# Kernel optimization log

Measured on AMD Instinct MI355X. Metric: run time of the kernel, lower is better.

## Reference

```python
import jax, jax.numpy as jnp
import numpy as np

B, T, F, H, OUT = 256, 256, 128, 1024, 128


def setup_inputs() -> dict:
    key = jax.random.key(0)
    ks = jax.random.split(key, 6)
    s_ih = 1.0 / np.sqrt(H)
    return {
        "x": jax.random.normal(ks[0], (B, T, F), dtype=jnp.float32),
        "h0": jnp.zeros((B, H), dtype=jnp.float32),
        "c0": jnp.zeros((B, H), dtype=jnp.float32),
        "W_ih": jax.random.normal(ks[1], (4 * H, F), dtype=jnp.float32) * s_ih,
        "W_hh": jax.random.normal(ks[2], (4 * H, H), dtype=jnp.float32) * s_ih,
        "b_ih": jax.random.normal(ks[3], (4 * H,), dtype=jnp.float32) * s_ih,
        "b_hh": jax.random.normal(ks[4], (4 * H,), dtype=jnp.float32) * s_ih,
        "W_fc": jax.random.normal(ks[5], (OUT, H), dtype=jnp.float32) * s_ih,
        "b_fc": jnp.zeros((OUT,), dtype=jnp.float32),
    }


def _lstm_scan(x, h0, c0, W_ih, W_hh, b_ih, b_hh):
    # Precompute input projections for all timesteps: [T, B, 4H]
    x_t = jnp.swapaxes(x, 0, 1)  # [T, B, F]
    x_proj = jnp.einsum('tbf,gf->tbg', x_t, W_ih) + b_ih + b_hh

    def step(carry, xp):
        h, c = carry
        gates = xp + h @ W_hh.T  # [B, 4H]
        i, f, g, o = jnp.split(gates, 4, axis=-1)  # PyTorch LSTMCell gate order
        i = jax.nn.sigmoid(i)
        f = jax.nn.sigmoid(f)
        g = jnp.tanh(g)
        o = jax.nn.sigmoid(o)
        c = f * c + i * g
        h = o * jnp.tanh(c)
        return (h, c), None

    (h, c), _ = jax.lax.scan(step, (h0, c0), x_proj)
    return h, c


def reference(x, h0, c0, W_ih, W_hh, b_ih, b_hh, W_fc, b_fc):
    h, c = _lstm_scan(x, h0, c0, W_ih, W_hh, b_ih, b_hh)
    sig_out = jax.nn.sigmoid(h)
    # Dropout is identity in eval/reference mode
    return sig_out @ W_fc.T + b_fc  # [B, OUT]
```

## Files before the change

### kernel.cpp

```cpp
#include <hip/hip_runtime.h>


typedef _Float16 f16x8 __attribute__((ext_vector_type(8)));
typedef float f32x16 __attribute__((ext_vector_type(16)));
typedef unsigned long long u64;

#define SCOPE_AGENT __HIP_MEMORY_SCOPE_AGENT

#define WS_WP    0ull
#define WS_BIAS  9437184ull
#define WS_XT    (WS_BIAS + 16384ull)
#define WS_HB    (WS_XT + 16777216ull)
#define WS_SIGH  (WS_HB + 4ull * 524288ull)
#define WS_BAR   (WS_SIGH + 1048576ull)

__device__ __forceinline__ unsigned short f2h(float f) {
  _Float16 h = (_Float16)f;
  return __builtin_bit_cast(unsigned short, h);
}

__device__ __forceinline__ float fast_sig(float x) {
  return __builtin_amdgcn_rcpf(1.f + __expf(-x));
}
__device__ __forceinline__ float fast_tanh(float x) {
  return __builtin_fmaf(2.f, fast_sig(2.f * x), -1.f);
}

__global__ void prep_pack(const float* __restrict__ W_ih, const float* __restrict__ W_hh,
                          const float* __restrict__ b_ih, const float* __restrict__ b_hh,
                          unsigned short* __restrict__ wp, float* __restrict__ bias) {
  unsigned i = blockIdx.x * 256u + threadIdx.x;
  if (i < 4718592u) {
    unsigned j = i & 7u;
    unsigned l = (i >> 3) & 63u;
    unsigned rest = i >> 9;
    unsigned q = rest % 18u;
    unsigned rest2 = rest / 18u;
    unsigned n = rest2 & 3u;
    unsigned rest3 = rest2 >> 2;
    unsigned w = rest3 & 3u;
    unsigned cg = rest3 >> 2;
    unsigned gcol = n * 1024u + cg * 32u + (l & 31u);
    unsigned khi = (l >> 5) * 8u + j;
    float v;
    if (q < 16u) {
      unsigned k = w * 256u + q * 16u + khi;
      v = W_hh[(size_t)gcol * 1024u + k];
    } else {
      unsigned k = w * 32u + (q - 16u) * 16u + khi;
      v = W_ih[(size_t)gcol * 128u + k];
    }
    wp[i] = f2h(v);
  }
  if (i < 4096u) bias[i] = b_ih[i] + b_hh[i];
}

__global__ void prep_misc(const float* __restrict__ x, const float* __restrict__ h0,
                          unsigned short* __restrict__ xT, unsigned short* __restrict__ hb0,
                          unsigned* __restrict__ bar) {
  unsigned i = blockIdx.x * 256u + threadIdx.x;
  if (i < 8388608u) {
    unsigned f = i & 127u;
    unsigned b = (i >> 7) & 255u;
    unsigned t = i >> 15;
    xT[i] = f2h(x[((size_t)b * 256u + t) * 128u + f]);
  }
  if (i < 262144u) hb0[i] = f2h(h0[i]);
  if (i < 768u) bar[i] = 0u;
}

__launch_bounds__(256, 1)
__global__ void lstm_main(const unsigned short* __restrict__ wp,
                          const float* __restrict__ bias,
                          const unsigned short* __restrict__ xT,
                          unsigned short* __restrict__ hb,
                          const float* __restrict__ c0,
                          float* __restrict__ sigh,
                          unsigned* __restrict__ bar) {
  extern __shared__ char lds[];
  float4* redv = (float4*)(lds + 65536);
  unsigned short* hst = (unsigned short*)(lds + 131072);

  const unsigned tid = threadIdx.x;
  const unsigned wg  = blockIdx.x;
  const unsigned w   = tid >> 6;
  const unsigned l   = tid & 63u;
  const unsigned rg  = wg >> 5;
  const unsigned cg  = wg & 31u;
  const unsigned lo5 = l & 31u;
  const unsigned hi  = l >> 5;

  int4 Braw[4][18];
  {
    const int4* wpv = (const int4*)wp;
    const unsigned wbase = (cg * 4u + w) * 4608u;
#pragma unroll
    for (int n = 0; n < 4; ++n) {
#pragma unroll
      for (int q = 0; q < 18; ++q) {
        Braw[n][q] = wpv[wbase + (unsigned)(n * 18 + q) * 64u + l];
      }
    }
  }

  float bias_v[4];
#pragma unroll
  for (int n = 0; n < 4; ++n) bias_v[n] = bias[(unsigned)n * 1024u + cg * 32u + lo5];

  const unsigned col = cg * 32u + lo5;
  float c_st[4];
  unsigned soff[4];
#pragma unroll
  for (int i = 0; i < 4; ++i) {
    unsigned r = rg * 32u + 8u * w + (unsigned)i + 4u * hi;
    soff[i] = r * 1024u + col;
    c_st[i] = c0[soff[i]];
  }

  const unsigned sgsrc0 = (rg * 32u + hi) * 2048u + w * 512u + lo5 * 16u;
  const unsigned sdst0  = w * 16384u + hi * 512u + lo5 * 16u;
  const unsigned fbase = w * 16384u + lo5 * 512u + hi * 16u;
  const unsigned fxor  = (lo5 & 7u) << 4;

  unsigned xb = ((rg * 32u + lo5) * 128u + w * 32u + hi * 8u) * 2u;

  const char* xbase = (const char*)xT;
  const char* hbase = (const char*)hb;
  unsigned* flags = &bar[rg * 32u];

  const unsigned srow = tid >> 3;
  const unsigned sseg = tid & 7u;
  const unsigned sgoff = (((rg * 32u + srow) * 1024u) + cg * 32u + sseg * 4u) * 2u;

  int4 xr[2];
  xr[0] = *(const int4*)(xbase + xb);
  xr[1] = *(const int4*)(xbase + xb + 32u);

  for (unsigned t = 0; t < 256u; ++t) {
    const char* hrd = hbase + ((t & 3u) * 524288u);
    char* hwr = (char*)hbase + (((t + 1u) & 3u) * 524288u);

    u64 sa[16], sb[16];
#pragma unroll
    for (int r = 0; r < 16; ++r) {
      const char* src = hrd + sgsrc0 + (unsigned)r * 4096u;
      sa[r] = __hip_atomic_load((const u64*)src,       __ATOMIC_RELAXED, SCOPE_AGENT);
      sb[r] = __hip_atomic_load((const u64*)(src + 8), __ATOMIC_RELAXED, SCOPE_AGENT);
    }

    f32x16 acc[4] = {};
#pragma unroll
    for (int qx = 0; qx < 2; ++qx) {
      f16x8 a = __builtin_bit_cast(f16x8, xr[qx]);
      acc[0] = __builtin_amdgcn_mfma_f32_32x32x16_f16(a, __builtin_bit_cast(f16x8, Braw[0][16 + qx]), acc[0], 0, 0, 0);
      acc[1] = __builtin_amdgcn_mfma_f32_32x32x16_f16(a, __builtin_bit_cast(f16x8, Braw[1][16 + qx]), acc[1], 0, 0, 0);
      acc[2] = __builtin_amdgcn_mfma_f32_32x32x16_f16(a, __builtin_bit_cast(f16x8, Braw[2][16 + qx]), acc[2], 0, 0, 0);
      acc[3] = __builtin_amdgcn_mfma_f32_32x32x16_f16(a, __builtin_bit_cast(f16x8, Braw[3][16 + qx]), acc[3], 0, 0, 0);
    }

#pragma unroll
    for (int r = 0; r < 16; ++r) {
      unsigned d = sdst0 + (unsigned)r * 1024u;
      unsigned a = d ^ (((d >> 9) & 7u) << 4);
      struct { u64 a, b; } p = { sa[r], sb[r] };
      *(int4*)(lds + a) = __builtin_bit_cast(int4, p);
    }
    asm volatile("s_waitcnt lgkmcnt(0)" ::: "memory");

#pragma unroll
    for (int q = 0; q < 16; ++q) {
      int4 av = *(const int4*)(lds + ((fbase + (unsigned)q * 32u) ^ fxor));
      f16x8 a = __builtin_bit_cast(f16x8, av);
      acc[0] = __builtin_amdgcn_mfma_f32_32x32x16_f16(a, __builtin_bit_cast(f16x8, Braw[0][q]), acc[0], 0, 0, 0);
      acc[1] = __builtin_amdgcn_mfma_f32_32x32x16_f16(a, __builtin_bit_cast(f16x8, Braw[1][q]), acc[1], 0, 0, 0);
      acc[2] = __builtin_amdgcn_mfma_f32_32x32x16_f16(a, __builtin_bit_cast(f16x8, Braw[2][q]), acc[2], 0, 0, 0);
      acc[3] = __builtin_amdgcn_mfma_f32_32x32x16_f16(a, __builtin_bit_cast(f16x8, Braw[3][q]), acc[3], 0, 0, 0);
    }

#pragma unroll
    for (int n = 0; n < 4; ++n) {
#pragma unroll
      for (int c = 0; c < 4; ++c) {
        float4 v;
        v.x = acc[n][4 * c + 0]; v.y = acc[n][4 * c + 1];
        v.z = acc[n][4 * c + 2]; v.w = acc[n][4 * c + 3];
        redv[((w * 4u + (unsigned)n) * 4u + (unsigned)c) * 64u + l] = v;
      }
    }
    __syncthreads();

    float gv[4][4];
#pragma unroll
    for (int n = 0; n < 4; ++n) {
      float4 s; s.x = bias_v[n]; s.y = bias_v[n]; s.z = bias_v[n]; s.w = bias_v[n];
#pragma unroll
      for (int wo = 0; wo < 4; ++wo) {
        float4 v = redv[(((unsigned)wo * 4u + (unsigned)n) * 4u + w) * 64u + l];
        s.x += v.x; s.y += v.y; s.z += v.z; s.w += v.w;
      }
      gv[n][0] = s.x; gv[n][1] = s.y; gv[n][2] = s.z; gv[n][3] = s.w;
    }

    const bool last = (t == 255u);
#pragma unroll
    for (int i = 0; i < 4; ++i) {
      float ig = fast_sig(gv[0][i]);
      float fg = fast_sig(gv[1][i]);
      float gg = fast_tanh(gv[2][i]);
      float og = fast_sig(gv[3][i]);
      float cc = fg * c_st[i] + ig * gg;
      c_st[i] = cc;
      float hh = og * fast_tanh(cc);
      hst[(8u * w + (unsigned)i + 4u * hi) * 32u + lo5] = f2h(hh);
      if (last) sigh[soff[i]] = fast_sig(hh);
    }

    if (!last) {
      __syncthreads();
      {
        u64 v = *(const u64*)(hst + srow * 32u + sseg * 4u);
        __hip_atomic_store((u64*)(hwr + sgoff), v, __ATOMIC_RELAXED, SCOPE_AGENT);
      }
      xb += 65536u;
      xr[0] = *(const int4*)(xbase + xb);
      xr[1] = *(const int4*)(xbase + xb + 32u);
      __syncthreads();
      if (tid == 0)
        __hip_atomic_store(&flags[cg], t + 1u, __ATOMIC_RELAXED, SCOPE_AGENT);
      {
        const unsigned tgt = t + 1u;
        const unsigned fidx = w * 8u + (l & 7u);
        for (;;) {
          unsigned f = __hip_atomic_load(&flags[fidx], __ATOMIC_RELAXED, SCOPE_AGENT);
          if (__all(l >= 8u || f >= tgt)) break;
          __builtin_amdgcn_s_sleep(1);
        }
      }
    }
  }
}

__global__ void final_fc(const float* __restrict__ sigh, const float* __restrict__ W_fc,
                         const float* __restrict__ b_fc, float* __restrict__ out) {
  unsigned b = blockIdx.x;
  unsigned o = threadIdx.x;
  const float* hrow = sigh + (size_t)b * 1024u;
  const float* wrow = W_fc + (size_t)o * 1024u;
  float acc = b_fc[o];
#pragma unroll 8
  for (unsigned k = 0; k < 1024u; k += 4u) {
    float4 hv = *(const float4*)(hrow + k);
    float4 wv = *(const float4*)(wrow + k);
    acc += hv.x * wv.x + hv.y * wv.y + hv.z * wv.z + hv.w * wv.w;
  }
  out[b * 128u + o] = acc;
}

extern "C" void kernel_launch(void* const* d_in, const int* in_sizes, int n_in,
                              void* d_out, int out_size, void* d_ws, size_t ws_size,
                              hipStream_t stream) {
  (void)in_sizes; (void)n_in; (void)out_size; (void)ws_size;
  const float* x    = (const float*)d_in[0];
  const float* h0   = (const float*)d_in[1];
  const float* c0   = (const float*)d_in[2];
  const float* W_ih = (const float*)d_in[3];
  const float* W_hh = (const float*)d_in[4];
  const float* b_ih = (const float*)d_in[5];
  const float* b_hh = (const float*)d_in[6];
  const float* W_fc = (const float*)d_in[7];
  const float* b_fc = (const float*)d_in[8];

  char* ws = (char*)d_ws;
  unsigned short* wp   = (unsigned short*)(ws + WS_WP);
  float*          bias = (float*)(ws + WS_BIAS);
  unsigned short* xT   = (unsigned short*)(ws + WS_XT);
  unsigned short* hb   = (unsigned short*)(ws + WS_HB);
  float*          sigh = (float*)(ws + WS_SIGH);
  unsigned*       bar  = (unsigned*)(ws + WS_BAR);
  float*          out  = (float*)d_out;

  prep_pack<<<18432, 256, 0, stream>>>(W_ih, W_hh, b_ih, b_hh, wp, bias);
  prep_misc<<<32768, 256, 0, stream>>>(x, h0, xT, hb, bar);
  lstm_main<<<256, 256, 133120, stream>>>(wp, bias, xT, hb, c0, sigh, bar);
  final_fc<<<256, 128, 0, stream>>>(sigh, W_fc, b_fc, out);
}
```

Before: 1.307 ms.

## Double waves per block, store h in MFMA fragment layout, drop LDS staging

Each workgroup now runs 8 waves instead of 4, so each wave handles half the K range with half the register-resident weights. The shared h buffer is stored directly in MFMA A-fragment layout, so waves load fragments from global memory without the LDS transpose, and the next fragments are prefetched while MFMAs run. The cross-wave reduction grows to 8 partials, and each thread applies the gate math to 2 rows. The flag polling also changes so all lanes check flags. The aim is more latency hiding and a shorter serial per-step path, at the cost of a larger reduction and smaller stores per thread.

```diff
diff --git a/kernel.cpp b/kernel.cpp
--- a/kernel.cpp
+++ b/kernel.cpp
@@ -4,6 +4,7 @@
 typedef _Float16 f16x8 __attribute__((ext_vector_type(8)));
 typedef float f32x16 __attribute__((ext_vector_type(16)));
 typedef unsigned long long u64;
+struct U128 { u64 a, b; };
 
 #define SCOPE_AGENT __HIP_MEMORY_SCOPE_AGENT
 
@@ -24,6 +25,13 @@
 }
 __device__ __forceinline__ float fast_tanh(float x) {
   return __builtin_fmaf(2.f, fast_sig(2.f * x), -1.f);
+}
+
+__device__ __forceinline__ int4 load_frag(const char* p) {
+  U128 u;
+  u.a = __hip_atomic_load((const u64*)p,       __ATOMIC_RELAXED, SCOPE_AGENT);
+  u.b = __hip_atomic_load((const u64*)(p + 8), __ATOMIC_RELAXED, SCOPE_AGENT);
+  return __builtin_bit_cast(int4, u);
 }
 
 __global__ void prep_pack(const float* __restrict__ W_ih, const float* __restrict__ W_hh,
@@ -34,21 +42,21 @@
     unsigned j = i & 7u;
     unsigned l = (i >> 3) & 63u;
     unsigned rest = i >> 9;
-    unsigned q = rest % 18u;
-    unsigned rest2 = rest / 18u;
+    unsigned q = rest % 9u;
+    unsigned rest2 = rest / 9u;
     unsigned n = rest2 & 3u;
     unsigned rest3 = rest2 >> 2;
-    unsigned w = rest3 & 3u;
-    unsigned cg = rest3 >> 2;
+    unsigned w = rest3 & 7u;
+    unsigned cg = rest3 >> 3;
     unsigned gcol = n * 1024u + cg * 32u + (l & 31u);
     unsigned khi = (l >> 5) * 8u + j;
     float v;
-    if (q < 16u) {
-      unsigned k = w * 256u + q * 16u + khi;
+    if (q < 8u) {
+      unsigned k = (w * 8u + q) * 16u + khi;
       v = W_hh[(size_t)gcol * 1024u + k];
     } else {
-      unsigned k = w * 32u + (q - 16u) * 16u + khi;
-      v = W_ih[(size_t)gcol * 128u + k];
+      unsigned f = w * 16u + khi;
+      v = W_ih[(size_t)gcol * 128u + f];
     }
     wp[i] = f2h(v);
   }
@@ -65,11 +73,19 @@
     unsigned t = i >> 15;
     xT[i] = f2h(x[((size_t)b * 256u + t) * 128u + f]);
   }
-  if (i < 262144u) hb0[i] = f2h(h0[i]);
+  if (i < 262144u) {
+    unsigned j = i & 7u;
+    unsigned l = (i >> 3) & 63u;
+    unsigned chunk = (i >> 9) & 63u;
+    unsigned rg = i >> 15;
+    unsigned row = rg * 32u + (l & 31u);
+    unsigned col = chunk * 16u + (l >> 5) * 8u + j;
+    hb0[i] = f2h(h0[row * 1024u + col]);
+  }
   if (i < 768u) bar[i] = 0u;
 }
 
-__launch_bounds__(256, 1)
+__launch_bounds__(512, 1)
 __global__ void lstm_main(const unsigned short* __restrict__ wp,
                           const float* __restrict__ bias,
                           const unsigned short* __restrict__ xT,
@@ -78,7 +94,8 @@
                           float* __restrict__ sigh,
                           unsigned* __restrict__ bar) {
   extern __shared__ char lds[];
-  float4* redv = (float4*)(lds + 65536);
+  float4* redv  = (float4*)lds;
+  float2* redv2 = (float2*)lds;
   unsigned short* hst = (unsigned short*)(lds + 131072);
 
   const unsigned tid = threadIdx.x;
@@ -89,16 +106,18 @@
   const unsigned cg  = wg & 31u;
   const unsigned lo5 = l & 31u;
   const unsigned hi  = l >> 5;
-
-  int4 Braw[4][18];
+  const unsigned cw    = w & 3u;
+  const unsigned ihalf = w >> 2;
+
+  int4 Braw[4][9];
   {
     const int4* wpv = (const int4*)wp;
-    const unsigned wbase = (cg * 4u + w) * 4608u;
+    const unsigned wbase = (cg * 8u + w) * 2304u;
 #pragma unroll
     for (int n = 0; n < 4; ++n) {
 #pragma unroll
-      for (int q = 0; q < 18; ++q) {
-        Braw[n][q] = wpv[wbase + (unsigned)(n * 18 + q) * 64u + l];
+      for (int q = 0; q < 9; ++q) {
+        Braw[n][q] = wpv[wbase + (unsigned)(n * 9 + q) * 64u + l];
       }
     }
   }
@@ -107,70 +126,54 @@
 #pragma unroll
   for (int n = 0; n < 4; ++n) bias_v[n] = bias[(unsigned)n * 1024u + cg * 32u + lo5];
 
-  const unsigned col = cg * 32u + lo5;
-  float c_st[4];
-  unsigned soff[4];
-#pragma unroll
-  for (int i = 0; i < 4; ++i) {
-    unsigned r = rg * 32u + 8u * w + (unsigned)i + 4u * hi;
-    soff[i] = r * 1024u + col;
+  const unsigned r0 = 8u * cw + 4u * hi + 2u * ihalf;
+  float c_st[2];
+  unsigned soff[2];
+#pragma unroll
+  for (int i = 0; i < 2; ++i) {
+    soff[i] = (rg * 32u + r0 + (unsigned)i) * 1024u + cg * 32u + lo5;
     c_st[i] = c0[soff[i]];
   }
 
-  const unsigned sgsrc0 = (rg * 32u + hi) * 2048u + w * 512u + lo5 * 16u;
-  const unsigned sdst0  = w * 16384u + hi * 512u + lo5 * 16u;
-  const unsigned fbase = w * 16384u + lo5 * 512u + hi * 16u;
-  const unsigned fxor  = (lo5 & 7u) << 4;
-
-  unsigned xb = ((rg * 32u + lo5) * 128u + w * 32u + hi * 8u) * 2u;
+  const unsigned fragbase = rg * 65536u + (w * 8u) * 1024u + l * 16u;
+  unsigned xb = (rg * 32u + lo5) * 256u + (w * 16u + hi * 8u) * 2u;
 
   const char* xbase = (const char*)xT;
   const char* hbase = (const char*)hb;
   unsigned* flags = &bar[rg * 32u];
 
-  const unsigned srow = tid >> 3;
-  const unsigned sseg = tid & 7u;
-  const unsigned sgoff = (((rg * 32u + srow) * 1024u) + cg * 32u + sseg * 4u) * 2u;
-
-  int4 xr[2];
-  xr[0] = *(const int4*)(xbase + xb);
-  xr[1] = *(const int4*)(xbase + xb + 32u);
+  const unsigned pq = tid >> 8;
+  const unsigned pl = (tid >> 2) & 63u;
+  const unsigned pp = tid & 3u;
+  const unsigned plc = pq * 16u + (pl >> 5) * 8u + pp * 2u;
+  const unsigned hst_rd = (pl & 31u) * 64u + plc * 2u;
+  const unsigned pw_off = rg * 65536u + (cg * 2u + pq) * 1024u + pl * 16u + pp * 4u;
+
+  int4 xr;
+  xr = *(const int4*)(xbase + xb);
 
   for (unsigned t = 0; t < 256u; ++t) {
     const char* hrd = hbase + ((t & 3u) * 524288u);
     char* hwr = (char*)hbase + (((t + 1u) & 3u) * 524288u);
 
-    u64 sa[16], sb[16];
-#pragma unroll
-    for (int r = 0; r < 16; ++r) {
-      const char* src = hrd + sgsrc0 + (unsigned)r * 4096u;
-      sa[r] = __hip_atomic_load((const u64*)src,       __ATOMIC_RELAXED, SCOPE_AGENT);
-      sb[r] = __hip_atomic_load((const u64*)(src + 8), __ATOMIC_RELAXED, SCOPE_AGENT);
-    }
+    int4 ah[4];
+#pragma unroll
+    for (int q = 0; q < 4; ++q)
+      ah[q] = load_frag(hrd + fragbase + (unsigned)q * 1024u);
 
     f32x16 acc[4] = {};
-#pragma unroll
-    for (int qx = 0; qx < 2; ++qx) {
-      f16x8 a = __builtin_bit_cast(f16x8, xr[qx]);
-      acc[0] = __builtin_amdgcn_mfma_f32_32x32x16_f16(a, __builtin_bit_cast(f16x8, Braw[0][16 + qx]), acc[0], 0, 0, 0);
-      acc[1] = __builtin_amdgcn_mfma_f32_32x32x16_f16(a, __builtin_bit_cast(f16x8, Braw[1][16 + qx]), acc[1], 0, 0, 0);
-      acc[2] = __builtin_amdgcn_mfma_f32_32x32x16_f16(a, __builtin_bit_cast(f16x8, Braw[2][16 + qx]), acc[2], 0, 0, 0);
-      acc[3] = __builtin_amdgcn_mfma_f32_32x32x16_f16(a, __builtin_bit_cast(f16x8, Braw[3][16 + qx]), acc[3], 0, 0, 0);
-    }
-
-#pragma unroll
-    for (int r = 0; r < 16; ++r) {
-      unsigned d = sdst0 + (unsigned)r * 1024u;
-      unsigned a = d ^ (((d >> 9) & 7u) << 4);
-      struct { u64 a, b; } p = { sa[r], sb[r] };
-      *(int4*)(lds + a) = __builtin_bit_cast(int4, p);
-    }
-    asm volatile("s_waitcnt lgkmcnt(0)" ::: "memory");
-
-#pragma unroll
-    for (int q = 0; q < 16; ++q) {
-      int4 av = *(const int4*)(lds + ((fbase + (unsigned)q * 32u) ^ fxor));
-      f16x8 a = __builtin_bit_cast(f16x8, av);
+    {
+      f16x8 a = __builtin_bit_cast(f16x8, xr);
+      acc[0] = __builtin_amdgcn_mfma_f32_32x32x16_f16(a, __builtin_bit_cast(f16x8, Braw[0][8]), acc[0], 0, 0, 0);
+      acc[1] = __builtin_amdgcn_mfma_f32_32x32x16_f16(a, __builtin_bit_cast(f16x8, Braw[1][8]), acc[1], 0, 0, 0);
+      acc[2] = __builtin_amdgcn_mfma_f32_32x32x16_f16(a, __builtin_bit_cast(f16x8, Braw[2][8]), acc[2], 0, 0, 0);
+      acc[3] = __builtin_amdgcn_mfma_f32_32x32x16_f16(a, __builtin_bit_cast(f16x8, Braw[3][8]), acc[3], 0, 0, 0);
+    }
+#pragma unroll
+    for (int q = 0; q < 8; ++q) {
+      f16x8 a = __builtin_bit_cast(f16x8, ah[q & 3]);
+      if (q + 4 < 8)
+        ah[q & 3] = load_frag(hrd + fragbase + (unsigned)(q + 4) * 1024u);
       acc[0] = __builtin_amdgcn_mfma_f32_32x32x16_f16(a, __builtin_bit_cast(f16x8, Braw[0][q]), acc[0], 0, 0, 0);
       acc[1] = __builtin_amdgcn_mfma_f32_32x32x16_f16(a, __builtin_bit_cast(f16x8, Braw[1][q]), acc[1], 0, 0, 0);
       acc[2] = __builtin_amdgcn_mfma_f32_32x32x16_f16(a, __builtin_bit_cast(f16x8, Braw[2][q]), acc[2], 0, 0, 0);
@@ -189,21 +192,21 @@
     }
     __syncthreads();
 
-    float gv[4][4];
+    float gv[4][2];
 #pragma unroll
     for (int n = 0; n < 4; ++n) {
-      float4 s; s.x = bias_v[n]; s.y = bias_v[n]; s.z = bias_v[n]; s.w = bias_v[n];
-#pragma unroll
-      for (int wo = 0; wo < 4; ++wo) {
-        float4 v = redv[(((unsigned)wo * 4u + (unsigned)n) * 4u + w) * 64u + l];
-        s.x += v.x; s.y += v.y; s.z += v.z; s.w += v.w;
-      }
-      gv[n][0] = s.x; gv[n][1] = s.y; gv[n][2] = s.z; gv[n][3] = s.w;
+      float s0 = bias_v[n], s1 = bias_v[n];
+#pragma unroll
+      for (int wo = 0; wo < 8; ++wo) {
+        float2 v = redv2[((((unsigned)wo * 4u + (unsigned)n) * 4u + cw) * 64u + l) * 2u + ihalf];
+        s0 += v.x; s1 += v.y;
+      }
+      gv[n][0] = s0; gv[n][1] = s1;
     }
 
     const bool last = (t == 255u);
 #pragma unroll
-    for (int i = 0; i < 4; ++i) {
+    for (int i = 0; i < 2; ++i) {
       float ig = fast_sig(gv[0][i]);
       float fg = fast_sig(gv[1][i]);
       float gg = fast_tanh(gv[2][i]);
@@ -211,28 +214,27 @@
       float cc = fg * c_st[i] + ig * gg;
       c_st[i] = cc;
       float hh = og * fast_tanh(cc);
-      hst[(8u * w + (unsigned)i + 4u * hi) * 32u + lo5] = f2h(hh);
+      hst[(r0 + (unsigned)i) * 32u + lo5] = f2h(hh);
       if (last) sigh[soff[i]] = fast_sig(hh);
     }
 
     if (!last) {
       __syncthreads();
       {
-        u64 v = *(const u64*)(hst + srow * 32u + sseg * 4u);
-        __hip_atomic_store((u64*)(hwr + sgoff), v, __ATOMIC_RELAXED, SCOPE_AGENT);
+        unsigned v = *(const unsigned*)((const char*)hst + hst_rd);
+        __hip_atomic_store((unsigned*)(hwr + pw_off), v, __ATOMIC_RELAXED, SCOPE_AGENT);
       }
       xb += 65536u;
-      xr[0] = *(const int4*)(xbase + xb);
-      xr[1] = *(const int4*)(xbase + xb + 32u);
+      xr = *(const int4*)(xbase + xb);
       __syncthreads();
       if (tid == 0)
         __hip_atomic_store(&flags[cg], t + 1u, __ATOMIC_RELAXED, SCOPE_AGENT);
       {
         const unsigned tgt = t + 1u;
-        const unsigned fidx = w * 8u + (l & 7u);
+        const unsigned fidx = w * 4u + (l & 3u);
         for (;;) {
           unsigned f = __hip_atomic_load(&flags[fidx], __ATOMIC_RELAXED, SCOPE_AGENT);
-          if (__all(l >= 8u || f >= tgt)) break;
+          if (__all(f >= tgt)) break;
           __builtin_amdgcn_s_sleep(1);
         }
       }
@@ -281,6 +283,6 @@
 
   prep_pack<<<18432, 256, 0, stream>>>(W_ih, W_hh, b_ih, b_hh, wp, bias);
   prep_misc<<<32768, 256, 0, stream>>>(x, h0, xT, hb, bar);
-  lstm_main<<<256, 256, 133120, stream>>>(wp, bias, xT, hb, c0, sigh, bar);
+  lstm_main<<<256, 512, 133120, stream>>>(wp, bias, xT, hb, c0, sigh, bar);
   final_fc<<<256, 128, 0, stream>>>(sigh, W_fc, b_fc, out);
 }
```

Result: slower. 1.587 ms (+21.4%).

## Store hidden state in MFMA fragment layout and load A operands directly from global

Applied to the files above, without the earlier changes.

The hidden-state exchange buffer is now written in the exact per-lane MFMA A-fragment order, so each wave loads its A operands straight from global memory with a 4-deep rolling prefetch instead of staging them through a swizzled LDS tile. This removes the LDS write/read round trip and the waitcnt on every timestep and halves the shared-memory allocation. The flag spin loop also drops the lane mask, which is harmless because lanes 8 and up reread the same flags. In exchange the MFMA chain now depends directly on global-load latency inside the loop, and the initial h0 packing is rewritten to match the new layout.

```diff
diff --git a/kernel.cpp b/kernel.cpp
--- a/kernel.cpp
+++ b/kernel.cpp
@@ -4,6 +4,7 @@
 typedef _Float16 f16x8 __attribute__((ext_vector_type(8)));
 typedef float f32x16 __attribute__((ext_vector_type(16)));
 typedef unsigned long long u64;
+struct U128 { u64 a, b; };
 
 #define SCOPE_AGENT __HIP_MEMORY_SCOPE_AGENT
 
@@ -24,6 +25,13 @@
 }
 __device__ __forceinline__ float fast_tanh(float x) {
   return __builtin_fmaf(2.f, fast_sig(2.f * x), -1.f);
+}
+
+__device__ __forceinline__ int4 load_frag(const char* p) {
+  U128 u;
+  u.a = __hip_atomic_load((const u64*)p,       __ATOMIC_RELAXED, SCOPE_AGENT);
+  u.b = __hip_atomic_load((const u64*)(p + 8), __ATOMIC_RELAXED, SCOPE_AGENT);
+  return __builtin_bit_cast(int4, u);
 }
 
 __global__ void prep_pack(const float* __restrict__ W_ih, const float* __restrict__ W_hh,
@@ -65,7 +73,15 @@
     unsigned t = i >> 15;
     xT[i] = f2h(x[((size_t)b * 256u + t) * 128u + f]);
   }
-  if (i < 262144u) hb0[i] = f2h(h0[i]);
+  if (i < 262144u) {
+    unsigned j = i & 7u;
+    unsigned l = (i >> 3) & 63u;
+    unsigned chunk = (i >> 9) & 63u;
+    unsigned rg = i >> 15;
+    unsigned row = rg * 32u + (l & 31u);
+    unsigned col = chunk * 16u + (l >> 5) * 8u + j;
+    hb0[i] = f2h(h0[row * 1024u + col]);
+  }
   if (i < 768u) bar[i] = 0u;
 }
 
@@ -78,8 +94,8 @@
                           float* __restrict__ sigh,
                           unsigned* __restrict__ bar) {
   extern __shared__ char lds[];
-  float4* redv = (float4*)(lds + 65536);
-  unsigned short* hst = (unsigned short*)(lds + 131072);
+  float4* redv = (float4*)lds;
+  unsigned short* hst = (unsigned short*)(lds + 65536);
 
   const unsigned tid = threadIdx.x;
   const unsigned wg  = blockIdx.x;
@@ -117,20 +133,19 @@
     c_st[i] = c0[soff[i]];
   }
 
-  const unsigned sgsrc0 = (rg * 32u + hi) * 2048u + w * 512u + lo5 * 16u;
-  const unsigned sdst0  = w * 16384u + hi * 512u + lo5 * 16u;
-  const unsigned fbase = w * 16384u + lo5 * 512u + hi * 16u;
-  const unsigned fxor  = (lo5 & 7u) << 4;
-
+  const unsigned fragbase = rg * 65536u + (w * 16u) * 1024u + l * 16u;
   unsigned xb = ((rg * 32u + lo5) * 128u + w * 32u + hi * 8u) * 2u;
 
   const char* xbase = (const char*)xT;
   const char* hbase = (const char*)hb;
   unsigned* flags = &bar[rg * 32u];
 
-  const unsigned srow = tid >> 3;
-  const unsigned sseg = tid & 7u;
-  const unsigned sgoff = (((rg * 32u + srow) * 1024u) + cg * 32u + sseg * 4u) * 2u;
+  const unsigned pq = tid >> 7;
+  const unsigned pl = (tid >> 1) & 63u;
+  const unsigned pp = tid & 1u;
+  const unsigned plc = pq * 16u + (pl >> 5) * 8u + pp * 4u;
+  const unsigned hst_rd = (pl & 31u) * 64u + plc * 2u;
+  const unsigned pw_off = rg * 65536u + (cg * 2u + pq) * 1024u + pl * 16u + pp * 8u;
 
   int4 xr[2];
   xr[0] = *(const int4*)(xbase + xb);
@@ -140,13 +155,10 @@
     const char* hrd = hbase + ((t & 3u) * 524288u);
     char* hwr = (char*)hbase + (((t + 1u) & 3u) * 524288u);
 
-    u64 sa[16], sb[16];
-#pragma unroll
-    for (int r = 0; r < 16; ++r) {
-      const char* src = hrd + sgsrc0 + (unsigned)r * 4096u;
-      sa[r] = __hip_atomic_load((const u64*)src,       __ATOMIC_RELAXED, SCOPE_AGENT);
-      sb[r] = __hip_atomic_load((const u64*)(src + 8), __ATOMIC_RELAXED, SCOPE_AGENT);
-    }
+    int4 ah[4];
+#pragma unroll
+    for (int q = 0; q < 4; ++q)
+      ah[q] = load_frag(hrd + fragbase + (unsigned)q * 1024u);
 
     f32x16 acc[4] = {};
 #pragma unroll
@@ -157,20 +169,11 @@
       acc[2] = __builtin_amdgcn_mfma_f32_32x32x16_f16(a, __builtin_bit_cast(f16x8, Braw[2][16 + qx]), acc[2], 0, 0, 0);
       acc[3] = __builtin_amdgcn_mfma_f32_32x32x16_f16(a, __builtin_bit_cast(f16x8, Braw[3][16 + qx]), acc[3], 0, 0, 0);
     }
-
-#pragma unroll
-    for (int r = 0; r < 16; ++r) {
-      unsigned d = sdst0 + (unsigned)r * 1024u;
-      unsigned a = d ^ (((d >> 9) & 7u) << 4);
-      struct { u64 a, b; } p = { sa[r], sb[r] };
-      *(int4*)(lds + a) = __builtin_bit_cast(int4, p);
-    }
-    asm volatile("s_waitcnt lgkmcnt(0)" ::: "memory");
-
 #pragma unroll
     for (int q = 0; q < 16; ++q) {
-      int4 av = *(const int4*)(lds + ((fbase + (unsigned)q * 32u) ^ fxor));
-      f16x8 a = __builtin_bit_cast(f16x8, av);
+      f16x8 a = __builtin_bit_cast(f16x8, ah[q & 3]);
+      if (q + 4 < 16)
+        ah[q & 3] = load_frag(hrd + fragbase + (unsigned)(q + 4) * 1024u);
       acc[0] = __builtin_amdgcn_mfma_f32_32x32x16_f16(a, __builtin_bit_cast(f16x8, Braw[0][q]), acc[0], 0, 0, 0);
       acc[1] = __builtin_amdgcn_mfma_f32_32x32x16_f16(a, __builtin_bit_cast(f16x8, Braw[1][q]), acc[1], 0, 0, 0);
       acc[2] = __builtin_amdgcn_mfma_f32_32x32x16_f16(a, __builtin_bit_cast(f16x8, Braw[2][q]), acc[2], 0, 0, 0);
@@ -218,8 +221,8 @@
     if (!last) {
       __syncthreads();
       {
-        u64 v = *(const u64*)(hst + srow * 32u + sseg * 4u);
-        __hip_atomic_store((u64*)(hwr + sgoff), v, __ATOMIC_RELAXED, SCOPE_AGENT);
+        u64 v = *(const u64*)((const char*)hst + hst_rd);
+        __hip_atomic_store((u64*)(hwr + pw_off), v, __ATOMIC_RELAXED, SCOPE_AGENT);
       }
       xb += 65536u;
       xr[0] = *(const int4*)(xbase + xb);
@@ -232,7 +235,7 @@
         const unsigned fidx = w * 8u + (l & 7u);
         for (;;) {
           unsigned f = __hip_atomic_load(&flags[fidx], __ATOMIC_RELAXED, SCOPE_AGENT);
-          if (__all(l >= 8u || f >= tgt)) break;
+          if (__all(f >= tgt)) break;
           __builtin_amdgcn_s_sleep(1);
         }
       }
@@ -281,6 +284,6 @@
 
   prep_pack<<<18432, 256, 0, stream>>>(W_ih, W_hh, b_ih, b_hh, wp, bias);
   prep_misc<<<32768, 256, 0, stream>>>(x, h0, xT, hb, bar);
-  lstm_main<<<256, 256, 133120, stream>>>(wp, bias, xT, hb, c0, sigh, bar);
+  lstm_main<<<256, 256, 67584, stream>>>(wp, bias, xT, hb, c0, sigh, bar);
   final_fc<<<256, 128, 0, stream>>>(sigh, W_fc, b_fc, out);
 }
```

Result: slower. 1.730 ms (+32.3%).

## Exchange hidden state between workgroups as 8-bit floats with scaled weights

Applied to the files above, without the earlier changes.

The per-step hidden-state exchange through global memory now uses a custom 8-bit float encoding (fp16 truncated to sign plus 7 bits, scaled by 1/256) instead of fp16. This halves the cross-workgroup traffic and the LDS staging. Weights are pre-scaled by 256 and the inputs by 1/256 so the products keep their magnitude, and the packed W_hh k-order is permuted to match the byte-interleaved dequantisation. The spin-wait condition is also simplified. The cost is lower precision in the recurrent state, which could push accuracy past tolerance, plus some extra ALU work to decode on every step.

```diff
diff --git a/kernel.cpp b/kernel.cpp
--- a/kernel.cpp
+++ b/kernel.cpp
@@ -11,7 +11,7 @@
 #define WS_BIAS  9437184ull
 #define WS_XT    (WS_BIAS + 16384ull)
 #define WS_HB    (WS_XT + 16777216ull)
-#define WS_SIGH  (WS_HB + 4ull * 524288ull)
+#define WS_SIGH  (WS_HB + 4ull * 262144ull)
 #define WS_BAR   (WS_SIGH + 1048576ull)
 
 __device__ __forceinline__ unsigned short f2h(float f) {
@@ -24,6 +24,25 @@
 }
 __device__ __forceinline__ float fast_tanh(float x) {
   return __builtin_fmaf(2.f, fast_sig(2.f * x), -1.f);
+}
+
+__device__ __forceinline__ unsigned char h_enc(float v) {
+  _Float16 gh = (_Float16)(v * 0.00390625f);
+  unsigned m = __builtin_bit_cast(unsigned short, gh);
+  unsigned r = m + 0x3fu + ((m >> 7) & 1u);
+  return (unsigned char)(((m >> 8) & 0x80u) | ((r >> 7) & 0x7fu));
+}
+
+__device__ __forceinline__ f16x8 dq(u64 v) {
+  unsigned w0 = (unsigned)v, w1 = (unsigned)(v >> 32);
+  unsigned e0 = w0 & 0x00ff00ffu, o0 = (w0 >> 8) & 0x00ff00ffu;
+  unsigned e1 = w1 & 0x00ff00ffu, o1 = (w1 >> 8) & 0x00ff00ffu;
+  int4 t;
+  t.x = (int)((e0 + (e0 & 0x00800080u)) << 7);
+  t.y = (int)((o0 + (o0 & 0x00800080u)) << 7);
+  t.z = (int)((e1 + (e1 & 0x00800080u)) << 7);
+  t.w = (int)((o1 + (o1 & 0x00800080u)) << 7);
+  return __builtin_bit_cast(f16x8, t);
 }
 
 __global__ void prep_pack(const float* __restrict__ W_ih, const float* __restrict__ W_hh,
@@ -41,31 +60,32 @@
     unsigned w = rest3 & 3u;
     unsigned cg = rest3 >> 2;
     unsigned gcol = n * 1024u + cg * 32u + (l & 31u);
-    unsigned khi = (l >> 5) * 8u + j;
+    unsigned khi = (l >> 5) * 8u;
     float v;
     if (q < 16u) {
-      unsigned k = w * 256u + q * 16u + khi;
+      unsigned pj = (0x75643120u >> (4u * j)) & 0xfu;
+      unsigned k = w * 256u + q * 16u + khi + pj;
       v = W_hh[(size_t)gcol * 1024u + k];
     } else {
-      unsigned k = w * 32u + (q - 16u) * 16u + khi;
+      unsigned k = w * 32u + (q - 16u) * 16u + khi + j;
       v = W_ih[(size_t)gcol * 128u + k];
     }
-    wp[i] = f2h(v);
+    wp[i] = f2h(v * 256.0f);
   }
   if (i < 4096u) bias[i] = b_ih[i] + b_hh[i];
 }
 
 __global__ void prep_misc(const float* __restrict__ x, const float* __restrict__ h0,
-                          unsigned short* __restrict__ xT, unsigned short* __restrict__ hb0,
+                          unsigned short* __restrict__ xT, unsigned char* __restrict__ hb0,
                           unsigned* __restrict__ bar) {
   unsigned i = blockIdx.x * 256u + threadIdx.x;
   if (i < 8388608u) {
     unsigned f = i & 127u;
     unsigned b = (i >> 7) & 255u;
     unsigned t = i >> 15;
-    xT[i] = f2h(x[((size_t)b * 256u + t) * 128u + f]);
-  }
-  if (i < 262144u) hb0[i] = f2h(h0[i]);
+    xT[i] = f2h(x[((size_t)b * 256u + t) * 128u + f] * 0.00390625f);
+  }
+  if (i < 262144u) hb0[i] = h_enc(h0[i]);
   if (i < 768u) bar[i] = 0u;
 }
 
@@ -73,13 +93,14 @@
 __global__ void lstm_main(const unsigned short* __restrict__ wp,
                           const float* __restrict__ bias,
                           const unsigned short* __restrict__ xT,
-                          unsigned short* __restrict__ hb,
+                          unsigned char* __restrict__ hb,
                           const float* __restrict__ c0,
                           float* __restrict__ sigh,
                           unsigned* __restrict__ bar) {
   extern __shared__ char lds[];
-  float4* redv = (float4*)(lds + 65536);
-  unsigned short* hst = (unsigned short*)(lds + 131072);
+  char* stg = lds;
+  float4* redv = (float4*)(lds + 32768);
+  unsigned char* hst8 = (unsigned char*)(lds + 98304);
 
   const unsigned tid = threadIdx.x;
   const unsigned wg  = blockIdx.x;
@@ -117,36 +138,34 @@
     c_st[i] = c0[soff[i]];
   }
 
-  const unsigned sgsrc0 = (rg * 32u + hi) * 2048u + w * 512u + lo5 * 16u;
-  const unsigned sdst0  = w * 16384u + hi * 512u + lo5 * 16u;
-  const unsigned fbase = w * 16384u + lo5 * 512u + hi * 16u;
-  const unsigned fxor  = (lo5 & 7u) << 4;
+  const unsigned sgsrc0 = (rg * 32u + hi) * 1024u + w * 256u + lo5 * 8u;
+  const unsigned sdst0  = w * 8192u + hi * 256u + lo5 * 8u;
+  const unsigned frb = w * 8192u + lo5 * 256u + hi * 8u;
+  const unsigned fxr = (lo5 & 7u) << 3;
 
   unsigned xb = ((rg * 32u + lo5) * 128u + w * 32u + hi * 8u) * 2u;
 
   const char* xbase = (const char*)xT;
-  const char* hbase = (const char*)hb;
+  char* hbase = (char*)hb;
   unsigned* flags = &bar[rg * 32u];
 
   const unsigned srow = tid >> 3;
   const unsigned sseg = tid & 7u;
-  const unsigned sgoff = (((rg * 32u + srow) * 1024u) + cg * 32u + sseg * 4u) * 2u;
+  const unsigned sgoff = (rg * 32u + srow) * 1024u + cg * 32u + sseg * 4u;
 
   int4 xr[2];
   xr[0] = *(const int4*)(xbase + xb);
   xr[1] = *(const int4*)(xbase + xb + 32u);
 
   for (unsigned t = 0; t < 256u; ++t) {
-    const char* hrd = hbase + ((t & 3u) * 524288u);
-    char* hwr = (char*)hbase + (((t + 1u) & 3u) * 524288u);
-
-    u64 sa[16], sb[16];
-#pragma unroll
-    for (int r = 0; r < 16; ++r) {
-      const char* src = hrd + sgsrc0 + (unsigned)r * 4096u;
-      sa[r] = __hip_atomic_load((const u64*)src,       __ATOMIC_RELAXED, SCOPE_AGENT);
-      sb[r] = __hip_atomic_load((const u64*)(src + 8), __ATOMIC_RELAXED, SCOPE_AGENT);
-    }
+    const char* hrd = hbase + ((t & 3u) * 262144u);
+    char* hwr = hbase + (((t + 1u) & 3u) * 262144u);
+
+    u64 sa[16];
+#pragma unroll
+    for (int r = 0; r < 16; ++r)
+      sa[r] = __hip_atomic_load((const u64*)(hrd + sgsrc0 + (unsigned)r * 2048u),
+                                __ATOMIC_RELAXED, SCOPE_AGENT);
 
     f32x16 acc[4] = {};
 #pragma unroll
@@ -160,17 +179,17 @@
 
 #pragma unroll
     for (int r = 0; r < 16; ++r) {
-      unsigned d = sdst0 + (unsigned)r * 1024u;
-      unsigned a = d ^ (((d >> 9) & 7u) << 4);
-      struct { u64 a, b; } p = { sa[r], sb[r] };
-      *(int4*)(lds + a) = __builtin_bit_cast(int4, p);
+      unsigned d = sdst0 + (unsigned)r * 512u;
+      unsigned a = d ^ (((d >> 8) & 7u) << 3);
+      *(u64*)(stg + a) = sa[r];
     }
     asm volatile("s_waitcnt lgkmcnt(0)" ::: "memory");
 
 #pragma unroll
     for (int q = 0; q < 16; ++q) {
-      int4 av = *(const int4*)(lds + ((fbase + (unsigned)q * 32u) ^ fxor));
-      f16x8 a = __builtin_bit_cast(f16x8, av);
+      unsigned a2 = (frb + (unsigned)q * 16u) ^ fxr;
+      u64 hv = *(const u64*)(stg + a2);
+      f16x8 a = dq(hv);
       acc[0] = __builtin_amdgcn_mfma_f32_32x32x16_f16(a, __builtin_bit_cast(f16x8, Braw[0][q]), acc[0], 0, 0, 0);
       acc[1] = __builtin_amdgcn_mfma_f32_32x32x16_f16(a, __builtin_bit_cast(f16x8, Braw[1][q]), acc[1], 0, 0, 0);
       acc[2] = __builtin_amdgcn_mfma_f32_32x32x16_f16(a, __builtin_bit_cast(f16x8, Braw[2][q]), acc[2], 0, 0, 0);
@@ -211,15 +230,15 @@
       float cc = fg * c_st[i] + ig * gg;
       c_st[i] = cc;
       float hh = og * fast_tanh(cc);
-      hst[(8u * w + (unsigned)i + 4u * hi) * 32u + lo5] = f2h(hh);
+      hst8[(8u * w + (unsigned)i + 4u * hi) * 32u + lo5] = h_enc(hh);
       if (last) sigh[soff[i]] = fast_sig(hh);
     }
 
     if (!last) {
       __syncthreads();
       {
-        u64 v = *(const u64*)(hst + srow * 32u + sseg * 4u);
-        __hip_atomic_store((u64*)(hwr + sgoff), v, __ATOMIC_RELAXED, SCOPE_AGENT);
+        unsigned v = *(const unsigned*)(hst8 + srow * 32u + sseg * 4u);
+        __hip_atomic_store((unsigned*)(hwr + sgoff), v, __ATOMIC_RELAXED, SCOPE_AGENT);
       }
       xb += 65536u;
       xr[0] = *(const int4*)(xbase + xb);
@@ -232,7 +251,7 @@
         const unsigned fidx = w * 8u + (l & 7u);
         for (;;) {
           unsigned f = __hip_atomic_load(&flags[fidx], __ATOMIC_RELAXED, SCOPE_AGENT);
-          if (__all(l >= 8u || f >= tgt)) break;
+          if (__all(f >= tgt)) break;
           __builtin_amdgcn_s_sleep(1);
         }
       }
@@ -274,13 +293,13 @@
   unsigned short* wp   = (unsigned short*)(ws + WS_WP);
   float*          bias = (float*)(ws + WS_BIAS);
   unsigned short* xT   = (unsigned short*)(ws + WS_XT);
-  unsigned short* hb   = (unsigned short*)(ws + WS_HB);
+  unsigned char*  hb   = (unsigned char*)(ws + WS_HB);
   float*          sigh = (float*)(ws + WS_SIGH);
   unsigned*       bar  = (unsigned*)(ws + WS_BAR);
   float*          out  = (float*)d_out;
 
   prep_pack<<<18432, 256, 0, stream>>>(W_ih, W_hh, b_ih, b_hh, wp, bias);
   prep_misc<<<32768, 256, 0, stream>>>(x, h0, xT, hb, bar);
-  lstm_main<<<256, 256, 133120, stream>>>(wp, bias, xT, hb, c0, sigh, bar);
+  lstm_main<<<256, 256, 99328, stream>>>(wp, bias, xT, hb, c0, sigh, bar);
   final_fc<<<256, 128, 0, stream>>>(sigh, W_fc, b_fc, out);
 }
```

Result: no change. 1.308 ms (+0.0%).
